# Optimization experiments

Hardware: AMD Instinct MI355X
Metric: run time of the kernel (lower is better)

## Reference

```python
import jax, jax.numpy as jnp
import numpy as np

EPS = 1e-05
DECAY = 0.99
K = 2048   # codebook_size
D = 256    # codebook_dim


def setup_inputs() -> dict:
    key = jax.random.key(0)
    k1, k2, k3 = jax.random.split(key, 3)
    hidden_states = jax.random.normal(k1, (16, 4096, D), dtype=jnp.float32)
    embed_sum = jax.random.normal(k2, (K, D), dtype=jnp.float32)
    cluster_usage = jax.random.uniform(k3, (K,), dtype=jnp.float32)
    return {"hidden_states": hidden_states, "embed_sum": embed_sum, "cluster_usage": cluster_usage}


def reference(hidden_states, embed_sum, cluster_usage):
    # embed property: embed_sum / clamp(cluster_usage, min=eps)
    embed = embed_sum / jnp.clip(cluster_usage, EPS, None)[:, None]  # [K, D]

    shape = hidden_states.shape
    flat = hidden_states.reshape(-1, shape[-1])  # [N, D]

    # quantize: cdist(p=2) + argmin. argmin over squared distances is identical
    # to argmin over euclidean distances, avoiding the sqrt.
    x2 = jnp.sum(flat * flat, axis=-1, keepdims=True)          # [N, 1]
    e2 = jnp.sum(embed * embed, axis=-1)[None, :]              # [1, K]
    d2 = x2 - 2.0 * (flat @ embed.T) + e2                      # [N, K]
    flat_ind = jnp.argmin(d2, axis=-1)                         # [N]

    embed_ind = flat_ind.reshape(shape[:-1])                   # [B, T]
    quantize = embed[flat_ind].reshape(shape)                  # [B, T, D]

    # training-path EMA accumulation (scatter_add -> segment_sum), functional form
    counts = jax.ops.segment_sum(jnp.ones_like(flat_ind, dtype=flat.dtype), flat_ind, num_segments=K)
    sums = jax.ops.segment_sum(flat, flat_ind, num_segments=K)  # [K, D]
    new_cluster_usage = cluster_usage * DECAY + counts * (1.0 - DECAY)
    new_embed_sum = embed_sum * DECAY + sums * (1.0 - DECAY)

    return quantize, embed_ind, new_cluster_usage, new_embed_sum
```

## Files before the change

kernel.cpp:

```cpp
#include <hip/hip_runtime.h>

#define EPSF 1e-5f
#define DECAYF 0.99f
#define KCODES 2048
#define DIM 256
#define CC 64

typedef _Float16 f16;
typedef f16 f16x8 __attribute__((ext_vector_type(8)));
typedef float f32x4 __attribute__((ext_vector_type(4)));

#define MFMA16(A, B, C) __builtin_amdgcn_mfma_f32_16x16x32_f16(A, B, C, 0, 0, 0)

#define OFF_AH 0
#define OFF_AL 16384
#define OFF_BH 32768
#define OFF_BL 49152

__device__ __forceinline__ void gload_lds16(const void* g, void* l) {
    __builtin_amdgcn_global_load_lds(
        (const __attribute__((address_space(1))) void*)g,
        (__attribute__((address_space(3))) void*)l, 16, 0, 0);
}

__global__ __launch_bounds__(256) void split_x_kernel(
    const float* __restrict__ x, f16* __restrict__ xh, f16* __restrict__ xl, int n8)
{
    int i = blockIdx.x * 256 + threadIdx.x;
    if (i >= n8) return;
    f32x4 v0 = ((const f32x4*)x)[2 * i];
    f32x4 v1 = ((const f32x4*)x)[2 * i + 1];
    f16x8 h, l;
    #pragma unroll
    for (int t = 0; t < 4; ++t) {
        f16 h0 = (f16)v0[t]; h[t] = h0; l[t] = (f16)(v0[t] - (float)h0);
        f16 h1 = (f16)v1[t]; h[t + 4] = h1; l[t + 4] = (f16)(v1[t] - (float)h1);
    }
    ((f16x8*)xh)[i] = h;
    ((f16x8*)xl)[i] = l;
}

__global__ __launch_bounds__(256) void prep_embed_kernel(
    const float* __restrict__ embed_sum, const float* __restrict__ usage,
    float* __restrict__ embed, f16* __restrict__ eh, f16* __restrict__ el,
    float* __restrict__ e2)
{
    int k = blockIdx.x;
    int d = threadIdx.x;
    float inv = 1.0f / fmaxf(usage[k], EPSF);
    float e = embed_sum[k * DIM + d] * inv;
    embed[k * DIM + d] = e;
    float ec = fminf(fmaxf(e, -65000.0f), 65000.0f);
    f16 h = (f16)ec;
    f16 l = (f16)(ec - (float)h);
    eh[k * DIM + d] = h;
    el[k * DIM + d] = l;
    float sq = e * e;
    #pragma unroll
    for (int off = 32; off > 0; off >>= 1) sq += __shfl_down(sq, off, 64);
    __shared__ float ws[4];
    if ((threadIdx.x & 63) == 0) ws[threadIdx.x >> 6] = sq;
    __syncthreads();
    if (threadIdx.x == 0) e2[k] = ws[0] + ws[1] + ws[2] + ws[3];
}

__global__ __launch_bounds__(512, 2) void argmin_kernel(
    const f16* __restrict__ xh, const f16* __restrict__ xl,
    const f16* __restrict__ eh, const f16* __restrict__ el,
    const float* __restrict__ e2, int* __restrict__ flat_ind, int* __restrict__ cnt)
{
    __shared__ __align__(1024) char lds[2 * 65536 + 8192];
    float* e2s = (float*)(lds + 131072);

    const int tid  = threadIdx.x;
    const int w    = tid >> 6, lane = tid & 63;
    const int l15  = lane & 15, l4 = lane >> 4;
    const int wm   = w >> 1, wn = w & 1;
    const int row0 = blockIdx.x * 256;
    const int gsw  = (lane & 3) ^ ((lane >> 3) & 3);
    const int lq   = lane >> 2;
    const int rslot = (l4 ^ ((l15 >> 1) & 3)) * 16;

    f32x4 acc[4][8];
    float best[16];
    int   bidx[16];
    #pragma unroll
    for (int t = 0; t < 16; ++t) { best[t] = 3.4e38f; bidx[t] = 0; }

    auto stageU = [&](const f16* rowbase, int koff, char* unit) {
        #pragma unroll
        for (int q = 0; q < 2; ++q) {
            const int r = w * 32 + q * 16 + lq;
            gload_lds16(rowbase + (size_t)r * DIM + koff + gsw * 8,
                        unit + w * 2048 + q * 1024 + lane * 16);
        }
    };

    ((f32x4*)e2s)[tid] = ((const f32x4*)e2)[tid];
    stageU(xh + (size_t)row0 * DIM, 0, lds + OFF_AH);
    stageU(xl + (size_t)row0 * DIM, 0, lds + OFF_AL);
    stageU(eh, 0, lds + OFF_BH);
    stageU(el, 0, lds + OFF_BL);

    for (int cc = 0; cc < CC; ++cc) {
        char* buf  = lds + (cc & 1) * 65536;
        char* nbuf = lds + ((cc + 1) & 1) * 65536;
        const int ct = cc >> 3, sd = cc & 7;
        const int nn = cc + 1;
        const int nct = nn >> 3, nsd = nn & 7;
        const bool more = (nn < CC);

        if (sd == 0) {
            #pragma unroll
            for (int i = 0; i < 4; ++i)
                #pragma unroll
                for (int j = 0; j < 8; ++j)
                    acc[i][j] = (f32x4){0.f, 0.f, 0.f, 0.f};
        }

        asm volatile("s_waitcnt vmcnt(0)" ::: "memory");
        __builtin_amdgcn_s_barrier();
        __builtin_amdgcn_sched_barrier(0);

        if (more) {
            stageU(xh + (size_t)row0 * DIM, nsd * 32, nbuf + OFF_AH);
            stageU(xl + (size_t)row0 * DIM, nsd * 32, nbuf + OFF_AL);
            stageU(eh + (size_t)(nct * 256) * DIM, nsd * 32, nbuf + OFF_BH);
            stageU(el + (size_t)(nct * 256) * DIM, nsd * 32, nbuf + OFF_BL);
        }

        f16x8 ah[4], al[4], bh[8], bl[8];
        #pragma unroll
        for (int i = 0; i < 4; ++i)
            ah[i] = *(const f16x8*)(buf + OFF_AH + (wm * 64 + i * 16 + l15) * 64 + rslot);
        #pragma unroll
        for (int j = 0; j < 8; ++j)
            bh[j] = *(const f16x8*)(buf + OFF_BH + (wn * 128 + j * 16 + l15) * 64 + rslot);
        #pragma unroll
        for (int i = 0; i < 4; ++i)
            al[i] = *(const f16x8*)(buf + OFF_AL + (wm * 64 + i * 16 + l15) * 64 + rslot);

        #pragma unroll
        for (int i = 0; i < 4; ++i)
            #pragma unroll
            for (int j = 0; j < 8; ++j)
                acc[i][j] = MFMA16(ah[i], bh[j], acc[i][j]);
        #pragma unroll
        for (int i = 0; i < 4; ++i)
            #pragma unroll
            for (int j = 0; j < 8; ++j)
                acc[i][j] = MFMA16(al[i], bh[j], acc[i][j]);

        #pragma unroll
        for (int j = 0; j < 8; ++j)
            bl[j] = *(const f16x8*)(buf + OFF_BL + (wn * 128 + j * 16 + l15) * 64 + rslot);
        #pragma unroll
        for (int i = 0; i < 4; ++i)
            #pragma unroll
            for (int j = 0; j < 8; ++j)
                acc[i][j] = MFMA16(ah[i], bl[j], acc[i][j]);

        if (sd == 7) {
            const int cbase = ct * 256 + wn * 128;
            #pragma unroll
            for (int j = 0; j < 8; ++j) {
                const int col = cbase + j * 16 + l15;
                const float e2v = e2s[col];
                #pragma unroll
                for (int i = 0; i < 4; ++i)
                    #pragma unroll
                    for (int r = 0; r < 4; ++r) {
                        float m = fmaf(-2.0f, acc[i][j][r], e2v);
                        const int tt_ = i * 4 + r;
                        if (m < best[tt_]) { best[tt_] = m; bidx[tt_] = col; }
                    }
            }
        }
    }

    __syncthreads();
    float* rv = (float*)lds;
    int*   ri = (int*)(lds + 4096);
    #pragma unroll
    for (int tt_ = 0; tt_ < 16; ++tt_) {
        float v = best[tt_];
        int  ix = bidx[tt_];
        #pragma unroll
        for (int m = 1; m <= 8; m <<= 1) {
            float ov = __shfl_xor(v, m, 64);
            int  oix = __shfl_xor(ix, m, 64);
            if (ov < v || (ov == v && oix < ix)) { v = ov; ix = oix; }
        }
        if (l15 == 0) {
            const int rl = wm * 64 + (tt_ >> 2) * 16 + l4 * 4 + (tt_ & 3);
            rv[rl * 2 + wn] = v;
            ri[rl * 2 + wn] = ix;
        }
    }
    __syncthreads();
    if (tid < 256) {
        float v0 = rv[tid * 2], v1 = rv[tid * 2 + 1];
        int   i0 = ri[tid * 2], i1 = ri[tid * 2 + 1];
        int ib = (v1 < v0 || (v1 == v0 && i1 < i0)) ? i1 : i0;
        flat_ind[row0 + tid] = ib;
        unsigned long long pending = ~0ULL;
        while (pending) {
            int leader = __ffsll((long long)pending) - 1;
            int lind = __shfl(ib, leader, 64);
            unsigned long long same = __ballot(ib == lind);
            if ((tid & 63) == leader) atomicAdd(&cnt[lind], (int)__popcll(same));
            pending &= ~same;
        }
    }
}

__global__ __launch_bounds__(256) void scan_kernel(
    const int* __restrict__ cnt, int* __restrict__ offs, int* __restrict__ cursor)
{
    __shared__ int ps[256];
    const int t = threadIdx.x;
    int pre[8], s = 0;
    #pragma unroll
    for (int j = 0; j < 8; ++j) { pre[j] = s; s += cnt[t * 8 + j]; }
    ps[t] = s;
    __syncthreads();
    for (int off = 1; off < 256; off <<= 1) {
        int v = (t >= off) ? ps[t - off] : 0;
        __syncthreads();
        ps[t] += v;
        __syncthreads();
    }
    int ex = (t > 0) ? ps[t - 1] : 0;
    #pragma unroll
    for (int j = 0; j < 8; ++j) {
        offs[t * 8 + j]   = ex + pre[j];
        cursor[t * 8 + j] = ex + pre[j];
    }
}

__global__ __launch_bounds__(256) void assign_kernel(
    const int* __restrict__ flat_ind, int* __restrict__ cursor,
    int* __restrict__ rowlist, int* __restrict__ codesorted)
{
    const int i    = blockIdx.x * 256 + threadIdx.x;
    const int lane = threadIdx.x & 63;
    const int ind  = flat_ind[i];
    int pos = 0;
    unsigned long long pending = ~0ULL;
    while (pending) {
        int leader = __ffsll((long long)pending) - 1;
        int lind = __shfl(ind, leader, 64);
        unsigned long long same = __ballot(ind == lind);
        if (ind == lind) {
            int base = 0;
            if (lane == leader) base = atomicAdd(&cursor[lind], (int)__popcll(same));
            base = __shfl(base, leader, 64);
            pos = base + (int)__popcll(same & ((1ULL << lane) - 1ULL));
        }
        pending &= ~same;
    }
    rowlist[pos] = i;
    codesorted[pos] = ind;
}

__global__ __launch_bounds__(256) void codesum_kernel(
    const float* __restrict__ x, const int* __restrict__ rowlist,
    const int* __restrict__ codesorted, float* __restrict__ sums)
{
    const int p0 = blockIdx.x * 64;
    __shared__ int rows[64], codes[64];
    if (threadIdx.x < 64) {
        rows[threadIdx.x]  = rowlist[p0 + threadIdx.x];
        codes[threadIdx.x] = codesorted[p0 + threadIdx.x];
    }
    __syncthreads();
    const int d = threadIdx.x;
    float acc = 0.f;
    int cur = codes[0];
    #pragma unroll 4
    for (int r = 0; r < 64; ++r) {
        const int c = codes[r];
        if (c != cur) {
            atomicAdd(&sums[(size_t)cur * DIM + d], acc);
            acc = 0.f; cur = c;
        }
        acc += x[(size_t)rows[r] * DIM + d];
    }
    atomicAdd(&sums[(size_t)cur * DIM + d], acc);
}

__global__ __launch_bounds__(256) void finalize_kernel(
    const float* __restrict__ embed_sum, const float* __restrict__ usage,
    const float* __restrict__ sums, const int* __restrict__ cnt,
    float* __restrict__ out_usage, float* __restrict__ out_es)
{
    const int k = blockIdx.x, d = threadIdx.x;
    out_es[k * DIM + d] = embed_sum[k * DIM + d] * DECAYF + sums[k * DIM + d] * (1.0f - DECAYF);
    if (d == 0)
        out_usage[k] = usage[k] * DECAYF + (float)cnt[k] * (1.0f - DECAYF);
}

__global__ __launch_bounds__(256) void quantize_kernel(
    const float* __restrict__ embed, const int* __restrict__ flat_ind,
    float* __restrict__ out_q, float* __restrict__ out_ind_f, int N)
{
    int i = blockIdx.x * 256 + threadIdx.x;
    int row = i >> 6, c4 = i & 63;
    int ind = flat_ind[row];
    ((f32x4*)out_q)[i] = ((const f32x4*)embed)[ind * 64 + c4];
    if (i < N) out_ind_f[i] = (float)flat_ind[i];
}

extern "C" void kernel_launch(void* const* d_in, const int* in_sizes, int n_in,
                              void* d_out, int out_size, void* d_ws, size_t ws_size,
                              hipStream_t stream)
{
    const float* hs        = (const float*)d_in[0];
    const float* embed_sum = (const float*)d_in[1];
    const float* usage     = (const float*)d_in[2];
    const int N = in_sizes[0] / DIM;

    float* ws_f      = (float*)d_ws;
    float* embed     = ws_f;
    float* e2        = embed + KCODES * DIM;
    float* sums      = e2 + KCODES;
    f16*   eh        = (f16*)(sums + KCODES * DIM);
    f16*   el        = eh + KCODES * DIM;
    int*   cnt       = (int*)(el + KCODES * DIM);
    int*   offs      = cnt + KCODES;
    int*   cursor    = offs + KCODES;
    int*   rowlist   = cursor + KCODES;
    int*   codesorted= rowlist + N;
    int*   flat_ind  = codesorted + N;

    float* out_q     = (float*)d_out;
    float* out_ind   = out_q + (size_t)N * DIM;
    float* out_usage = out_ind + N;
    float* out_es    = out_usage + KCODES;

    f16* xh = (f16*)out_q;
    f16* xl = xh + (size_t)N * DIM;

    hipMemsetAsync(cnt, 0, KCODES * sizeof(int), stream);
    hipMemsetAsync(sums, 0, (size_t)KCODES * DIM * sizeof(float), stream);

    split_x_kernel<<<(N * DIM / 8 + 255) / 256, 256, 0, stream>>>(hs, xh, xl, N * DIM / 8);
    prep_embed_kernel<<<KCODES, 256, 0, stream>>>(embed_sum, usage, embed, eh, el, e2);
    argmin_kernel<<<N / 256, 512, 0, stream>>>(xh, xl, eh, el, e2, flat_ind, cnt);
    scan_kernel<<<1, 256, 0, stream>>>(cnt, offs, cursor);
    assign_kernel<<<N / 256, 256, 0, stream>>>(flat_ind, cursor, rowlist, codesorted);
    codesum_kernel<<<N / 64, 256, 0, stream>>>(hs, rowlist, codesorted, sums);
    finalize_kernel<<<KCODES, 256, 0, stream>>>(embed_sum, usage, sums, cnt, out_usage, out_es);
    quantize_kernel<<<N * DIM / 4 / 256, 256, 0, stream>>>(embed, flat_ind, out_q, out_ind, N);
}
```

Before: 289.0 us.

## Halve argmin tile to 128x128, fuse prep and finalize kernels, merge memsets

```diff
diff --git a/kernel.cpp b/kernel.cpp
--- a/kernel.cpp
+++ b/kernel.cpp
@@ -4,18 +4,18 @@
 #define DECAYF 0.99f
 #define KCODES 2048
 #define DIM 256
-#define CC 64
+#define CC 128
+#define BUFSZ 32768
+#define OFF_AH 0
+#define OFF_AL 8192
+#define OFF_BH 16384
+#define OFF_BL 24576
 
 typedef _Float16 f16;
 typedef f16 f16x8 __attribute__((ext_vector_type(8)));
 typedef float f32x4 __attribute__((ext_vector_type(4)));
 
 #define MFMA16(A, B, C) __builtin_amdgcn_mfma_f32_16x16x32_f16(A, B, C, 0, 0, 0)
-
-#define OFF_AH 0
-#define OFF_AL 16384
-#define OFF_BH 32768
-#define OFF_BL 49152
 
 __device__ __forceinline__ void gload_lds16(const void* g, void* l) {
     __builtin_amdgcn_global_load_lds(
@@ -23,88 +23,83 @@
         (__attribute__((address_space(3))) void*)l, 16, 0, 0);
 }
 
-__global__ __launch_bounds__(256) void split_x_kernel(
-    const float* __restrict__ x, f16* __restrict__ xh, f16* __restrict__ xl, int n8)
-{
-    int i = blockIdx.x * 256 + threadIdx.x;
-    if (i >= n8) return;
-    f32x4 v0 = ((const f32x4*)x)[2 * i];
-    f32x4 v1 = ((const f32x4*)x)[2 * i + 1];
-    f16x8 h, l;
-    #pragma unroll
-    for (int t = 0; t < 4; ++t) {
-        f16 h0 = (f16)v0[t]; h[t] = h0; l[t] = (f16)(v0[t] - (float)h0);
-        f16 h1 = (f16)v1[t]; h[t + 4] = h1; l[t + 4] = (f16)(v1[t] - (float)h1);
-    }
-    ((f16x8*)xh)[i] = h;
-    ((f16x8*)xl)[i] = l;
-}
-
-__global__ __launch_bounds__(256) void prep_embed_kernel(
+__global__ __launch_bounds__(256) void split_prep_kernel(
+    const float* __restrict__ x, f16* __restrict__ xh, f16* __restrict__ xl, int nsplit,
     const float* __restrict__ embed_sum, const float* __restrict__ usage,
     float* __restrict__ embed, f16* __restrict__ eh, f16* __restrict__ el,
     float* __restrict__ e2)
 {
-    int k = blockIdx.x;
-    int d = threadIdx.x;
-    float inv = 1.0f / fmaxf(usage[k], EPSF);
-    float e = embed_sum[k * DIM + d] * inv;
-    embed[k * DIM + d] = e;
-    float ec = fminf(fmaxf(e, -65000.0f), 65000.0f);
-    f16 h = (f16)ec;
-    f16 l = (f16)(ec - (float)h);
-    eh[k * DIM + d] = h;
-    el[k * DIM + d] = l;
-    float sq = e * e;
-    #pragma unroll
-    for (int off = 32; off > 0; off >>= 1) sq += __shfl_down(sq, off, 64);
-    __shared__ float ws[4];
-    if ((threadIdx.x & 63) == 0) ws[threadIdx.x >> 6] = sq;
-    __syncthreads();
-    if (threadIdx.x == 0) e2[k] = ws[0] + ws[1] + ws[2] + ws[3];
-}
-
-__global__ __launch_bounds__(512, 2) void argmin_kernel(
+    if ((int)blockIdx.x < nsplit) {
+        int i = blockIdx.x * 256 + threadIdx.x;
+        f32x4 v0 = ((const f32x4*)x)[2 * i];
+        f32x4 v1 = ((const f32x4*)x)[2 * i + 1];
+        f16x8 h, l;
+        #pragma unroll
+        for (int t = 0; t < 4; ++t) {
+            f16 h0 = (f16)v0[t]; h[t] = h0; l[t] = (f16)(v0[t] - (float)h0);
+            f16 h1 = (f16)v1[t]; h[t + 4] = h1; l[t + 4] = (f16)(v1[t] - (float)h1);
+        }
+        ((f16x8*)xh)[i] = h;
+        ((f16x8*)xl)[i] = l;
+    } else {
+        int k = blockIdx.x - nsplit;
+        int d = threadIdx.x;
+        float inv = 1.0f / fmaxf(usage[k], EPSF);
+        float e = embed_sum[k * DIM + d] * inv;
+        embed[k * DIM + d] = e;
+        float ec = fminf(fmaxf(e, -65000.0f), 65000.0f);
+        f16 h = (f16)ec;
+        f16 l = (f16)(ec - (float)h);
+        eh[k * DIM + d] = h;
+        el[k * DIM + d] = l;
+        float sq = e * e;
+        #pragma unroll
+        for (int off = 32; off > 0; off >>= 1) sq += __shfl_down(sq, off, 64);
+        __shared__ float ws[4];
+        if ((threadIdx.x & 63) == 0) ws[threadIdx.x >> 6] = sq;
+        __syncthreads();
+        if (threadIdx.x == 0) e2[k] = ws[0] + ws[1] + ws[2] + ws[3];
+    }
+}
+
+__global__ __launch_bounds__(512, 4) void argmin_kernel(
     const f16* __restrict__ xh, const f16* __restrict__ xl,
     const f16* __restrict__ eh, const f16* __restrict__ el,
     const float* __restrict__ e2, int* __restrict__ flat_ind, int* __restrict__ cnt)
 {
-    __shared__ __align__(1024) char lds[2 * 65536 + 8192];
-    float* e2s = (float*)(lds + 131072);
+    __shared__ __align__(1024) char lds[2 * BUFSZ + 8192];
+    float* e2s = (float*)(lds + 2 * BUFSZ);
 
     const int tid  = threadIdx.x;
     const int w    = tid >> 6, lane = tid & 63;
     const int l15  = lane & 15, l4 = lane >> 4;
     const int wm   = w >> 1, wn = w & 1;
-    const int row0 = blockIdx.x * 256;
+    const int row0 = blockIdx.x * 128;
     const int gsw  = (lane & 3) ^ ((lane >> 3) & 3);
     const int lq   = lane >> 2;
     const int rslot = (l4 ^ ((l15 >> 1) & 3)) * 16;
 
-    f32x4 acc[4][8];
-    float best[16];
-    int   bidx[16];
+    f32x4 acc[2][4];
+    float best[8];
+    int   bidx[8];
     #pragma unroll
-    for (int t = 0; t < 16; ++t) { best[t] = 3.4e38f; bidx[t] = 0; }
+    for (int t = 0; t < 8; ++t) { best[t] = 3.4e38f; bidx[t] = 0; }
 
     auto stageU = [&](const f16* rowbase, int koff, char* unit) {
-        #pragma unroll
-        for (int q = 0; q < 2; ++q) {
-            const int r = w * 32 + q * 16 + lq;
-            gload_lds16(rowbase + (size_t)r * DIM + koff + gsw * 8,
-                        unit + w * 2048 + q * 1024 + lane * 16);
-        }
+        const int r = w * 16 + lq;
+        gload_lds16(rowbase + (size_t)r * DIM + koff + gsw * 8, unit + w * 1024);
     };
 
     ((f32x4*)e2s)[tid] = ((const f32x4*)e2)[tid];
+    asm volatile("s_waitcnt lgkmcnt(0)" ::: "memory");
     stageU(xh + (size_t)row0 * DIM, 0, lds + OFF_AH);
     stageU(xl + (size_t)row0 * DIM, 0, lds + OFF_AL);
     stageU(eh, 0, lds + OFF_BH);
     stageU(el, 0, lds + OFF_BL);
 
     for (int cc = 0; cc < CC; ++cc) {
-        char* buf  = lds + (cc & 1) * 65536;
-        char* nbuf = lds + ((cc + 1) & 1) * 65536;
+        char* buf  = lds + (cc & 1) * BUFSZ;
+        char* nbuf = lds + ((cc + 1) & 1) * BUFSZ;
         const int ct = cc >> 3, sd = cc & 7;
         const int nn = cc + 1;
         const int nct = nn >> 3, nsd = nn & 7;
@@ -112,9 +107,9 @@
 
         if (sd == 0) {
             #pragma unroll
-            for (int i = 0; i < 4; ++i)
+            for (int i = 0; i < 2; ++i)
                 #pragma unroll
-                for (int j = 0; j < 8; ++j)
+                for (int j = 0; j < 4; ++j)
                     acc[i][j] = (f32x4){0.f, 0.f, 0.f, 0.f};
         }
 
@@ -125,54 +120,52 @@
         if (more) {
             stageU(xh + (size_t)row0 * DIM, nsd * 32, nbuf + OFF_AH);
             stageU(xl + (size_t)row0 * DIM, nsd * 32, nbuf + OFF_AL);
-            stageU(eh + (size_t)(nct * 256) * DIM, nsd * 32, nbuf + OFF_BH);
-            stageU(el + (size_t)(nct * 256) * DIM, nsd * 32, nbuf + OFF_BL);
-        }
-
-        f16x8 ah[4], al[4], bh[8], bl[8];
-        #pragma unroll
-        for (int i = 0; i < 4; ++i)
-            ah[i] = *(const f16x8*)(buf + OFF_AH + (wm * 64 + i * 16 + l15) * 64 + rslot);
-        #pragma unroll
-        for (int j = 0; j < 8; ++j)
-            bh[j] = *(const f16x8*)(buf + OFF_BH + (wn * 128 + j * 16 + l15) * 64 + rslot);
-        #pragma unroll
-        for (int i = 0; i < 4; ++i)
-            al[i] = *(const f16x8*)(buf + OFF_AL + (wm * 64 + i * 16 + l15) * 64 + rslot);
-
-        #pragma unroll
-        for (int i = 0; i < 4; ++i)
-            #pragma unroll
-            for (int j = 0; j < 8; ++j)
+            stageU(eh + (size_t)(nct * 128) * DIM, nsd * 32, nbuf + OFF_BH);
+            stageU(el + (size_t)(nct * 128) * DIM, nsd * 32, nbuf + OFF_BL);
+        }
+
+        f16x8 ah[2], al[2], bh[4], bl[4];
+        #pragma unroll
+        for (int i = 0; i < 2; ++i)
+            ah[i] = *(const f16x8*)(buf + OFF_AH + (wm * 32 + i * 16 + l15) * 64 + rslot);
+        #pragma unroll
+        for (int j = 0; j < 4; ++j)
+            bh[j] = *(const f16x8*)(buf + OFF_BH + (wn * 64 + j * 16 + l15) * 64 + rslot);
+        #pragma unroll
+        for (int i = 0; i < 2; ++i)
+            #pragma unroll
+            for (int j = 0; j < 4; ++j)
                 acc[i][j] = MFMA16(ah[i], bh[j], acc[i][j]);
         #pragma unroll
-        for (int i = 0; i < 4; ++i)
-            #pragma unroll
-            for (int j = 0; j < 8; ++j)
+        for (int i = 0; i < 2; ++i)
+            al[i] = *(const f16x8*)(buf + OFF_AL + (wm * 32 + i * 16 + l15) * 64 + rslot);
+        #pragma unroll
+        for (int i = 0; i < 2; ++i)
+            #pragma unroll
+            for (int j = 0; j < 4; ++j)
                 acc[i][j] = MFMA16(al[i], bh[j], acc[i][j]);
-
-        #pragma unroll
-        for (int j = 0; j < 8; ++j)
-            bl[j] = *(const f16x8*)(buf + OFF_BL + (wn * 128 + j * 16 + l15) * 64 + rslot);
-        #pragma unroll
-        for (int i = 0; i < 4; ++i)
-            #pragma unroll
-            for (int j = 0; j < 8; ++j)
+        #pragma unroll
+        for (int j = 0; j < 4; ++j)
+            bl[j] = *(const f16x8*)(buf + OFF_BL + (wn * 64 + j * 16 + l15) * 64 + rslot);
+        #pragma unroll
+        for (int i = 0; i < 2; ++i)
+            #pragma unroll
+            for (int j = 0; j < 4; ++j)
                 acc[i][j] = MFMA16(ah[i], bl[j], acc[i][j]);
 
         if (sd == 7) {
-            const int cbase = ct * 256 + wn * 128;
-            #pragma unroll
-            for (int j = 0; j < 8; ++j) {
+            const int cbase = ct * 128 + wn * 64;
+            #pragma unroll
+            for (int j = 0; j < 4; ++j) {
                 const int col = cbase + j * 16 + l15;
                 const float e2v = e2s[col];
                 #pragma unroll
-                for (int i = 0; i < 4; ++i)
+                for (int i = 0; i < 2; ++i)
                     #pragma unroll
                     for (int r = 0; r < 4; ++r) {
                         float m = fmaf(-2.0f, acc[i][j][r], e2v);
-                        const int tt_ = i * 4 + r;
-                        if (m < best[tt_]) { best[tt_] = m; bidx[tt_] = col; }
+                        const int t = i * 4 + r;
+                        if (m < best[t]) { best[t] = m; bidx[t] = col; }
                     }
             }
         }
@@ -180,11 +173,11 @@
 
     __syncthreads();
     float* rv = (float*)lds;
-    int*   ri = (int*)(lds + 4096);
+    int*   ri = (int*)(lds + 1024);
     #pragma unroll
-    for (int tt_ = 0; tt_ < 16; ++tt_) {
-        float v = best[tt_];
-        int  ix = bidx[tt_];
+    for (int t = 0; t < 8; ++t) {
+        float v = best[t];
+        int  ix = bidx[t];
         #pragma unroll
         for (int m = 1; m <= 8; m <<= 1) {
             float ov = __shfl_xor(v, m, 64);
@@ -192,13 +185,13 @@
             if (ov < v || (ov == v && oix < ix)) { v = ov; ix = oix; }
         }
         if (l15 == 0) {
-            const int rl = wm * 64 + (tt_ >> 2) * 16 + l4 * 4 + (tt_ & 3);
+            const int rl = wm * 32 + (t >> 2) * 16 + l4 * 4 + (t & 3);
             rv[rl * 2 + wn] = v;
             ri[rl * 2 + wn] = ix;
         }
     }
     __syncthreads();
-    if (tid < 256) {
+    if (tid < 128) {
         float v0 = rv[tid * 2], v1 = rv[tid * 2 + 1];
         int   i0 = ri[tid * 2], i1 = ri[tid * 2 + 1];
         int ib = (v1 < v0 || (v1 == v0 && i1 < i0)) ? i1 : i0;
@@ -289,26 +282,25 @@
     atomicAdd(&sums[(size_t)cur * DIM + d], acc);
 }
 
-__global__ __launch_bounds__(256) void finalize_kernel(
+__global__ __launch_bounds__(256) void quant_final_kernel(
+    const float* __restrict__ embed, const int* __restrict__ flat_ind,
+    float* __restrict__ out_q, float* __restrict__ out_ind_f, int N, int nq,
     const float* __restrict__ embed_sum, const float* __restrict__ usage,
     const float* __restrict__ sums, const int* __restrict__ cnt,
     float* __restrict__ out_usage, float* __restrict__ out_es)
 {
-    const int k = blockIdx.x, d = threadIdx.x;
-    out_es[k * DIM + d] = embed_sum[k * DIM + d] * DECAYF + sums[k * DIM + d] * (1.0f - DECAYF);
-    if (d == 0)
-        out_usage[k] = usage[k] * DECAYF + (float)cnt[k] * (1.0f - DECAYF);
-}
-
-__global__ __launch_bounds__(256) void quantize_kernel(
-    const float* __restrict__ embed, const int* __restrict__ flat_ind,
-    float* __restrict__ out_q, float* __restrict__ out_ind_f, int N)
-{
-    int i = blockIdx.x * 256 + threadIdx.x;
-    int row = i >> 6, c4 = i & 63;
-    int ind = flat_ind[row];
-    ((f32x4*)out_q)[i] = ((const f32x4*)embed)[ind * 64 + c4];
-    if (i < N) out_ind_f[i] = (float)flat_ind[i];
+    if ((int)blockIdx.x < nq) {
+        int i = blockIdx.x * 256 + threadIdx.x;
+        int row = i >> 6, c4 = i & 63;
+        int ind = flat_ind[row];
+        ((f32x4*)out_q)[i] = ((const f32x4*)embed)[ind * 64 + c4];
+        if (i < N) out_ind_f[i] = (float)flat_ind[i];
+    } else {
+        const int k = blockIdx.x - nq, d = threadIdx.x;
+        out_es[k * DIM + d] = embed_sum[k * DIM + d] * DECAYF + sums[k * DIM + d] * (1.0f - DECAYF);
+        if (d == 0)
+            out_usage[k] = usage[k] * DECAYF + (float)cnt[k] * (1.0f - DECAYF);
+    }
 }
 
 extern "C" void kernel_launch(void* const* d_in, const int* in_sizes, int n_in,
@@ -324,10 +316,10 @@
     float* embed     = ws_f;
     float* e2        = embed + KCODES * DIM;
     float* sums      = e2 + KCODES;
-    f16*   eh        = (f16*)(sums + KCODES * DIM);
+    int*   cnt       = (int*)(sums + KCODES * DIM);
+    f16*   eh        = (f16*)(cnt + KCODES);
     f16*   el        = eh + KCODES * DIM;
-    int*   cnt       = (int*)(el + KCODES * DIM);
-    int*   offs      = cnt + KCODES;
+    int*   offs      = (int*)(el + KCODES * DIM);
     int*   cursor    = offs + KCODES;
     int*   rowlist   = cursor + KCODES;
     int*   codesorted= rowlist + N;
@@ -341,15 +333,17 @@
     f16* xh = (f16*)out_q;
     f16* xl = xh + (size_t)N * DIM;
 
-    hipMemsetAsync(cnt, 0, KCODES * sizeof(int), stream);
-    hipMemsetAsync(sums, 0, (size_t)KCODES * DIM * sizeof(float), stream);
-
-    split_x_kernel<<<(N * DIM / 8 + 255) / 256, 256, 0, stream>>>(hs, xh, xl, N * DIM / 8);
-    prep_embed_kernel<<<KCODES, 256, 0, stream>>>(embed_sum, usage, embed, eh, el, e2);
-    argmin_kernel<<<N / 256, 512, 0, stream>>>(xh, xl, eh, el, e2, flat_ind, cnt);
+    hipMemsetAsync(sums, 0, (size_t)(KCODES * DIM + KCODES) * sizeof(float), stream);
+
+    const int nsplit = N * DIM / 8 / 256;
+    split_prep_kernel<<<nsplit + KCODES, 256, 0, stream>>>(
+        hs, xh, xl, nsplit, embed_sum, usage, embed, eh, el, e2);
+    argmin_kernel<<<N / 128, 512, 0, stream>>>(xh, xl, eh, el, e2, flat_ind, cnt);
     scan_kernel<<<1, 256, 0, stream>>>(cnt, offs, cursor);
     assign_kernel<<<N / 256, 256, 0, stream>>>(flat_ind, cursor, rowlist, codesorted);
     codesum_kernel<<<N / 64, 256, 0, stream>>>(hs, rowlist, codesorted, sums);
-    finalize_kernel<<<KCODES, 256, 0, stream>>>(embed_sum, usage, sums, cnt, out_usage, out_es);
-    quantize_kernel<<<N * DIM / 4 / 256, 256, 0, stream>>>(embed, flat_ind, out_q, out_ind, N);
-}
+    const int nq = N * DIM / 4 / 256;
+    quant_final_kernel<<<nq + KCODES, 256, 0, stream>>>(
+        embed, flat_ind, out_q, out_ind, N, nq,
+        embed_sum, usage, sums, cnt, out_usage, out_es);
+}
```

Result: slower. 311.1 us (+7.7%).

## Prune unreachable codebook entries via norm bound and fuse quantize into codesum

Applied to the files above, without the earlier changes.

```diff
diff --git a/kernel.cpp b/kernel.cpp
--- a/kernel.cpp
+++ b/kernel.cpp
@@ -4,7 +4,6 @@
 #define DECAYF 0.99f
 #define KCODES 2048
 #define DIM 256
-#define CC 64
 
 typedef _Float16 f16;
 typedef f16 f16x8 __attribute__((ext_vector_type(8)));
@@ -23,55 +22,133 @@
         (__attribute__((address_space(3))) void*)l, 16, 0, 0);
 }
 
-__global__ __launch_bounds__(256) void split_x_kernel(
-    const float* __restrict__ x, f16* __restrict__ xh, f16* __restrict__ xl, int n8)
-{
-    int i = blockIdx.x * 256 + threadIdx.x;
-    if (i >= n8) return;
-    f32x4 v0 = ((const f32x4*)x)[2 * i];
-    f32x4 v1 = ((const f32x4*)x)[2 * i + 1];
-    f16x8 h, l;
-    #pragma unroll
-    for (int t = 0; t < 4; ++t) {
-        f16 h0 = (f16)v0[t]; h[t] = h0; l[t] = (f16)(v0[t] - (float)h0);
-        f16 h1 = (f16)v1[t]; h[t + 4] = h1; l[t + 4] = (f16)(v1[t] - (float)h1);
-    }
-    ((f16x8*)xh)[i] = h;
-    ((f16x8*)xl)[i] = l;
-}
-
-__global__ __launch_bounds__(256) void prep_embed_kernel(
+__global__ __launch_bounds__(256) void split_prep_kernel(
+    const float* __restrict__ x, f16* __restrict__ xh, f16* __restrict__ xl, int nsplit,
     const float* __restrict__ embed_sum, const float* __restrict__ usage,
     float* __restrict__ embed, f16* __restrict__ eh, f16* __restrict__ el,
-    float* __restrict__ e2)
-{
-    int k = blockIdx.x;
-    int d = threadIdx.x;
-    float inv = 1.0f / fmaxf(usage[k], EPSF);
-    float e = embed_sum[k * DIM + d] * inv;
-    embed[k * DIM + d] = e;
-    float ec = fminf(fmaxf(e, -65000.0f), 65000.0f);
-    f16 h = (f16)ec;
-    f16 l = (f16)(ec - (float)h);
-    eh[k * DIM + d] = h;
-    el[k * DIM + d] = l;
-    float sq = e * e;
-    #pragma unroll
-    for (int off = 32; off > 0; off >>= 1) sq += __shfl_down(sq, off, 64);
-    __shared__ float ws[4];
-    if ((threadIdx.x & 63) == 0) ws[threadIdx.x >> 6] = sq;
+    float* __restrict__ e2, unsigned* __restrict__ maxx2_u, unsigned* __restrict__ mine2_u)
+{
+    if ((int)blockIdx.x < nsplit) {
+        int i = blockIdx.x * 256 + threadIdx.x;
+        f32x4 v0 = ((const f32x4*)x)[2 * i];
+        f32x4 v1 = ((const f32x4*)x)[2 * i + 1];
+        f16x8 h, l;
+        float p = 0.f;
+        #pragma unroll
+        for (int t = 0; t < 4; ++t) {
+            f16 h0 = (f16)v0[t]; h[t] = h0; l[t] = (f16)(v0[t] - (float)h0);
+            f16 h1 = (f16)v1[t]; h[t + 4] = h1; l[t + 4] = (f16)(v1[t] - (float)h1);
+            p += v0[t] * v0[t] + v1[t] * v1[t];
+        }
+        ((f16x8*)xh)[i] = h;
+        ((f16x8*)xl)[i] = l;
+        #pragma unroll
+        for (int m = 1; m <= 16; m <<= 1) p += __shfl_xor(p, m, 64);
+        float q = fmaxf(p, __shfl_xor(p, 32, 64));
+        __shared__ float wmax[4];
+        if ((threadIdx.x & 63) == 0) wmax[threadIdx.x >> 6] = q;
+        __syncthreads();
+        if (threadIdx.x == 0) {
+            float bm = fmaxf(fmaxf(wmax[0], wmax[1]), fmaxf(wmax[2], wmax[3]));
+            atomicMax(maxx2_u, __float_as_uint(bm));
+        }
+    } else {
+        int k = blockIdx.x - nsplit;
+        int d = threadIdx.x;
+        float inv = 1.0f / fmaxf(usage[k], EPSF);
+        float e = embed_sum[k * DIM + d] * inv;
+        embed[k * DIM + d] = e;
+        float ec = fminf(fmaxf(e, -65000.0f), 65000.0f);
+        f16 h = (f16)ec;
+        f16 l = (f16)(ec - (float)h);
+        eh[k * DIM + d] = h;
+        el[k * DIM + d] = l;
+        float sq = e * e;
+        #pragma unroll
+        for (int off = 32; off > 0; off >>= 1) sq += __shfl_down(sq, off, 64);
+        __shared__ float ws[4];
+        if ((threadIdx.x & 63) == 0) ws[threadIdx.x >> 6] = sq;
+        __syncthreads();
+        if (threadIdx.x == 0) {
+            float s = ws[0] + ws[1] + ws[2] + ws[3];
+            e2[k] = s;
+            atomicMin(mine2_u, __float_as_uint(s));
+        }
+    }
+}
+
+__global__ __launch_bounds__(256) void compactA_kernel(
+    const float* __restrict__ e2, const unsigned* __restrict__ maxx2_u,
+    const unsigned* __restrict__ mine2_u, int* __restrict__ cpos,
+    float* __restrict__ ce2, int* __restrict__ cmap, int* __restrict__ meta)
+{
+    __shared__ int ps[256];
+    const int t = threadIdx.x;
+    const float T0 = 2.0f * sqrtf(__uint_as_float(*maxx2_u)) + sqrtf(__uint_as_float(*mine2_u));
+    const float T = T0 * T0 * 1.0002f + 1.0f;
+    int flag[8], pre[8], s = 0;
+    float ev[8];
+    #pragma unroll
+    for (int j = 0; j < 8; ++j) {
+        ev[j] = e2[t * 8 + j];
+        flag[j] = (ev[j] <= T) ? 1 : 0;
+        pre[j] = s; s += flag[j];
+    }
+    ps[t] = s;
     __syncthreads();
-    if (threadIdx.x == 0) e2[k] = ws[0] + ws[1] + ws[2] + ws[3];
+    for (int off = 1; off < 256; off <<= 1) {
+        int v = (t >= off) ? ps[t - off] : 0;
+        __syncthreads();
+        ps[t] += v;
+        __syncthreads();
+    }
+    const int ex = (t > 0) ? ps[t - 1] : 0;
+    const int kp = ps[255];
+    #pragma unroll
+    for (int j = 0; j < 8; ++j) {
+        const int k = t * 8 + j;
+        if (flag[j]) {
+            const int p = ex + pre[j];
+            cpos[k] = p;
+            ce2[p] = ev[j];
+            cmap[p] = k;
+        } else cpos[k] = -1;
+    }
+    for (int j = t; j < KCODES; j += 256)
+        if (j >= kp) { ce2[j] = 3.4e38f; cmap[j] = 0; }
+    if (t == 0) { meta[0] = kp; meta[1] = (kp + 255) & ~255; }
+}
+
+__global__ __launch_bounds__(256) void compactB_kernel(
+    const f16* __restrict__ eh, const f16* __restrict__ el, const int* __restrict__ cpos,
+    const int* __restrict__ meta, f16* __restrict__ ceh, f16* __restrict__ cel)
+{
+    const int b = blockIdx.x, t = threadIdx.x;
+    if (b < KCODES) {
+        const int p = cpos[b];
+        if (p >= 0) {
+            ceh[p * DIM + t] = eh[b * DIM + t];
+            cel[p * DIM + t] = el[b * DIM + t];
+        }
+    } else {
+        const int slot = meta[0] + (b - KCODES);
+        if (slot < meta[1]) {
+            ceh[slot * DIM + t] = (f16)0.f;
+            cel[slot * DIM + t] = (f16)0.f;
+        }
+    }
 }
 
 __global__ __launch_bounds__(512, 2) void argmin_kernel(
     const f16* __restrict__ xh, const f16* __restrict__ xl,
-    const f16* __restrict__ eh, const f16* __restrict__ el,
-    const float* __restrict__ e2, int* __restrict__ flat_ind, int* __restrict__ cnt)
+    const f16* __restrict__ ceh, const f16* __restrict__ cel,
+    const float* __restrict__ ce2, const int* __restrict__ cmap,
+    const int* __restrict__ meta, int* __restrict__ flat_ind, int* __restrict__ cnt)
 {
     __shared__ __align__(1024) char lds[2 * 65536 + 8192];
     float* e2s = (float*)(lds + 131072);
 
+    const int ncc = meta[1] >> 5;
     const int tid  = threadIdx.x;
     const int w    = tid >> 6, lane = tid & 63;
     const int l15  = lane & 15, l4 = lane >> 4;
@@ -96,19 +173,19 @@
         }
     };
 
-    ((f32x4*)e2s)[tid] = ((const f32x4*)e2)[tid];
+    ((f32x4*)e2s)[tid] = ((const f32x4*)ce2)[tid];
     stageU(xh + (size_t)row0 * DIM, 0, lds + OFF_AH);
     stageU(xl + (size_t)row0 * DIM, 0, lds + OFF_AL);
-    stageU(eh, 0, lds + OFF_BH);
-    stageU(el, 0, lds + OFF_BL);
-
-    for (int cc = 0; cc < CC; ++cc) {
+    stageU(ceh, 0, lds + OFF_BH);
+    stageU(cel, 0, lds + OFF_BL);
+
+    for (int cc = 0; cc < ncc; ++cc) {
         char* buf  = lds + (cc & 1) * 65536;
         char* nbuf = lds + ((cc + 1) & 1) * 65536;
         const int ct = cc >> 3, sd = cc & 7;
         const int nn = cc + 1;
         const int nct = nn >> 3, nsd = nn & 7;
-        const bool more = (nn < CC);
+        const bool more = (nn < ncc);
 
         if (sd == 0) {
             #pragma unroll
@@ -125,8 +202,8 @@
         if (more) {
             stageU(xh + (size_t)row0 * DIM, nsd * 32, nbuf + OFF_AH);
             stageU(xl + (size_t)row0 * DIM, nsd * 32, nbuf + OFF_AL);
-            stageU(eh + (size_t)(nct * 256) * DIM, nsd * 32, nbuf + OFF_BH);
-            stageU(el + (size_t)(nct * 256) * DIM, nsd * 32, nbuf + OFF_BL);
+            stageU(ceh + (size_t)(nct * 256) * DIM, nsd * 32, nbuf + OFF_BH);
+            stageU(cel + (size_t)(nct * 256) * DIM, nsd * 32, nbuf + OFF_BL);
         }
 
         f16x8 ah[4], al[4], bh[8], bl[8];
@@ -201,7 +278,8 @@
     if (tid < 256) {
         float v0 = rv[tid * 2], v1 = rv[tid * 2 + 1];
         int   i0 = ri[tid * 2], i1 = ri[tid * 2 + 1];
-        int ib = (v1 < v0 || (v1 == v0 && i1 < i0)) ? i1 : i0;
+        int ibc = (v1 < v0 || (v1 == v0 && i1 < i0)) ? i1 : i0;
+        int ib = cmap[ibc];
         flat_ind[row0 + tid] = ib;
         unsigned long long pending = ~0ULL;
         while (pending) {
@@ -265,7 +343,9 @@
 
 __global__ __launch_bounds__(256) void codesum_kernel(
     const float* __restrict__ x, const int* __restrict__ rowlist,
-    const int* __restrict__ codesorted, float* __restrict__ sums)
+    const int* __restrict__ codesorted, float* __restrict__ sums,
+    const float* __restrict__ embed, float* __restrict__ out_q,
+    float* __restrict__ out_ind_f)
 {
     const int p0 = blockIdx.x * 64;
     __shared__ int rows[64], codes[64];
@@ -280,11 +360,14 @@
     #pragma unroll 4
     for (int r = 0; r < 64; ++r) {
         const int c = codes[r];
+        const int row = rows[r];
         if (c != cur) {
             atomicAdd(&sums[(size_t)cur * DIM + d], acc);
             acc = 0.f; cur = c;
         }
-        acc += x[(size_t)rows[r] * DIM + d];
+        acc += x[(size_t)row * DIM + d];
+        out_q[(size_t)row * DIM + d] = embed[(size_t)c * DIM + d];
+        if (d == 0) out_ind_f[row] = (float)c;
     }
     atomicAdd(&sums[(size_t)cur * DIM + d], acc);
 }
@@ -300,17 +383,6 @@
         out_usage[k] = usage[k] * DECAYF + (float)cnt[k] * (1.0f - DECAYF);
 }
 
-__global__ __launch_bounds__(256) void quantize_kernel(
-    const float* __restrict__ embed, const int* __restrict__ flat_ind,
-    float* __restrict__ out_q, float* __restrict__ out_ind_f, int N)
-{
-    int i = blockIdx.x * 256 + threadIdx.x;
-    int row = i >> 6, c4 = i & 63;
-    int ind = flat_ind[row];
-    ((f32x4*)out_q)[i] = ((const f32x4*)embed)[ind * 64 + c4];
-    if (i < N) out_ind_f[i] = (float)flat_ind[i];
-}
-
 extern "C" void kernel_launch(void* const* d_in, const int* in_sizes, int n_in,
                               void* d_out, int out_size, void* d_ws, size_t ws_size,
                               hipStream_t stream)
@@ -324,10 +396,17 @@
     float* embed     = ws_f;
     float* e2        = embed + KCODES * DIM;
     float* sums      = e2 + KCODES;
-    f16*   eh        = (f16*)(sums + KCODES * DIM);
+    int*   cnt       = (int*)(sums + KCODES * DIM);
+    f16*   eh        = (f16*)(cnt + KCODES);
     f16*   el        = eh + KCODES * DIM;
-    int*   cnt       = (int*)(el + KCODES * DIM);
-    int*   offs      = cnt + KCODES;
+    f16*   ceh       = el + KCODES * DIM;
+    f16*   cel       = ceh + KCODES * DIM;
+    float* ce2       = (float*)(cel + KCODES * DIM);
+    int*   cmap      = (int*)(ce2 + KCODES);
+    int*   cpos      = cmap + KCODES;
+    int*   meta      = cpos + KCODES;
+    unsigned* stats  = (unsigned*)(meta + 16);
+    int*   offs      = (int*)(stats + 2);
     int*   cursor    = offs + KCODES;
     int*   rowlist   = cursor + KCODES;
     int*   codesorted= rowlist + N;
@@ -341,15 +420,21 @@
     f16* xh = (f16*)out_q;
     f16* xl = xh + (size_t)N * DIM;
 
-    hipMemsetAsync(cnt, 0, KCODES * sizeof(int), stream);
-    hipMemsetAsync(sums, 0, (size_t)KCODES * DIM * sizeof(float), stream);
-
-    split_x_kernel<<<(N * DIM / 8 + 255) / 256, 256, 0, stream>>>(hs, xh, xl, N * DIM / 8);
-    prep_embed_kernel<<<KCODES, 256, 0, stream>>>(embed_sum, usage, embed, eh, el, e2);
-    argmin_kernel<<<N / 256, 512, 0, stream>>>(xh, xl, eh, el, e2, flat_ind, cnt);
+    hipMemsetAsync(sums, 0, (size_t)(KCODES * DIM + KCODES) * sizeof(float), stream);
+    hipMemsetAsync(stats, 0x00, 4, stream);
+    hipMemsetAsync(stats + 1, 0xFF, 4, stream);
+
+    const int nsplit = N * DIM / 8 / 256;
+    split_prep_kernel<<<nsplit + KCODES, 256, 0, stream>>>(
+        hs, xh, xl, nsplit, embed_sum, usage, embed, eh, el, e2, stats, stats + 1);
+    compactA_kernel<<<1, 256, 0, stream>>>(e2, stats, stats + 1, cpos, ce2, cmap, meta);
+    compactB_kernel<<<KCODES + 256, 256, 0, stream>>>(eh, el, cpos, meta, ceh, cel);
+    argmin_kernel<<<N / 256, 512, 0, stream>>>(xh, xl, ceh, cel, ce2, cmap, meta,
+                                               flat_ind, cnt);
     scan_kernel<<<1, 256, 0, stream>>>(cnt, offs, cursor);
     assign_kernel<<<N / 256, 256, 0, stream>>>(flat_ind, cursor, rowlist, codesorted);
-    codesum_kernel<<<N / 64, 256, 0, stream>>>(hs, rowlist, codesorted, sums);
-    finalize_kernel<<<KCODES, 256, 0, stream>>>(embed_sum, usage, sums, cnt, out_usage, out_es);
-    quantize_kernel<<<N * DIM / 4 / 256, 256, 0, stream>>>(embed, flat_ind, out_q, out_ind, N);
-}
+    codesum_kernel<<<N / 64, 256, 0, stream>>>(hs, rowlist, codesorted, sums,
+                                               embed, out_q, out_ind);
+    finalize_kernel<<<KCODES, 256, 0, stream>>>(embed_sum, usage, sums, cnt,
+                                                out_usage, out_es);
+}
```

Result: slower. 353.2 us (+22.2%).
